# Kernel optimization log

Measured on AMD Instinct MI355X. Metric: run time of the kernel, lower is better.

Reference implementation:

```python
import jax, jax.numpy as jnp
import numpy as np

THETA = 10.0      # neuron['theta']
TAU_SR = 10.0     # neuron['tauSr']
TAU_REF = 1.0     # neuron['tauRef']
SCALE_REF = 2.0   # neuron['scaleRef']
TAU_RHO = 1.0     # neuron['tauRho']
SCALE_RHO = 1.0   # neuron['scaleRho']
EPS = 0.01        # kernel truncation epsilon
TS = 1.0          # simulation['Ts']
T_SAMPLE = 256    # time steps == seq_len (forward sets tSample = embed_out.size(1))


def _alpha_kernel(tau, mult):
    # slayerPytorch _calculateAlphaKernel: mult * t/tau * exp(1 - t/tau), truncated
    ker = []
    for t in np.arange(0.0, T_SAMPLE * TS, TS):
        v = mult * t / tau * np.exp(1.0 - t / tau)
        if abs(v) < EPS and t > tau:
            break
        ker.append(v)
    return np.asarray(ker, dtype=np.float32)


def psp(x, srm_kernel):
    # Causal temporal filter: out[t] = Ts * sum_k srm[k] * x[t-k];  x: (B, C, T)
    B, C, T = x.shape
    K = srm_kernel.shape[0]
    lhs = x.reshape(B * C, 1, T)
    rhs = srm_kernel[::-1].reshape(1, 1, K)  # reverse: correlation -> convolution
    out = jax.lax.conv_general_dilated(lhs, rhs, (1,), [(K - 1, 0)])
    return out.reshape(B, C, T) * TS


def _spike_scan(u, ref_kernel):
    # Sequential threshold with refractory feedback (SLAYER getSpikes). u: (B, C, T)
    B, C, T = u.shape
    future = ref_kernel[1:]  # ref_kernel[0] == 0, so spike at t only affects t+1..
    R = future.shape[0]

    def step(r, u_t):
        m = u_t + r[..., 0]                       # membrane incl. past refractory
        s = (m >= THETA).astype(u.dtype)
        r = jnp.concatenate([r[..., 1:], jnp.zeros_like(r[..., :1])], axis=-1)
        r = r + s[..., None] * future             # schedule refractory response
        return r, (s, m)

    r0 = jnp.zeros((B, C, R), u.dtype)
    _, (s, m) = jax.lax.scan(step, r0, jnp.moveaxis(u, -1, 0))
    return jnp.moveaxis(s, 0, -1), jnp.moveaxis(m, 0, -1)


@jax.custom_vjp
def spike(u, ref_kernel):
    return _spike_scan(u, ref_kernel)[0]


def _spike_fwd(u, ref_kernel):
    s, m = _spike_scan(u, ref_kernel)
    return s, (m, ref_kernel)


def _spike_bwd(res, g):
    # SLAYER surrogate gradient: straight-through pdf on post-refractory membrane
    m, ref_kernel = res
    tau = TAU_RHO * THETA
    pdf = (SCALE_RHO / tau) * jnp.exp(-jnp.abs(m - THETA) / tau)
    return g * pdf, jnp.zeros_like(ref_kernel)


spike.defvjp(_spike_fwd, _spike_bwd)


def setup_inputs() -> dict:
    key = jax.random.key(0)
    k1, k2, k3, k4 = jax.random.split(key, 4)
    VOCAB, EMB, HID, OUT, B = 50000, 300, 512, 10, 64
    feed_data = jax.random.randint(k1, (B, T_SAMPLE), 0, VOCAB)
    emb_weight = jax.random.normal(k2, (VOCAB, EMB), jnp.float32)
    W1 = jax.random.normal(k3, (HID, EMB), jnp.float32) * (4.0 / np.sqrt(EMB))
    W2 = jax.random.normal(k4, (OUT, HID), jnp.float32) * (4.0 / np.sqrt(HID))
    return {
        "feed_data": feed_data,
        "emb_weight": emb_weight,
        "W1": W1,
        "W2": W2,
        "srm_kernel": jnp.asarray(_alpha_kernel(TAU_SR, 1.0)),
        "ref_kernel": jnp.asarray(_alpha_kernel(TAU_REF, -SCALE_REF * THETA)),
    }


def reference(feed_data, emb_weight, W1, W2, srm_kernel, ref_kernel):
    x = emb_weight[feed_data]                 # (B, T, E); dropout = identity (eval)
    x = jnp.transpose(x, (0, 2, 1))           # (B, E, T) -- transpose(1,2)
    h = jnp.einsum('he,bet->bht', W1, x)      # slayer.dense == 1x1x1 conv3d, no bias
    h = spike(psp(h, srm_kernel), ref_kernel)
    o = jnp.einsum('oh,bht->bot', W2, h)
    return spike(psp(o, srm_kernel), ref_kernel)  # (B, OUT, T)
```

## Files before the change

### kernel.cpp

```cpp
#include <hip/hip_runtime.h>

#define BB    64
#define TT    256
#define EMBD  300
#define HIDD  512
#define OUTC  10
#define THETA 10.0
#define FUTN  12
#define KSMAX 80
#define HSTRIDE 344

__device__ __forceinline__ int hswz(int tt) { return tt ^ ((tt >> 4) & 7); }

__global__ __launch_bounds__(256)
void prep_kernel(const int* __restrict__ feed, const float* __restrict__ emb,
                 const float* __restrict__ W2, float* __restrict__ xg,
                 double* __restrict__ w2d)
{
    if (blockIdx.y == 8) {
        const int k = blockIdx.x * 256 + threadIdx.x;
        if (k < OUTC * HIDD) w2d[k] = (double)W2[k];
        return;
    }
    __shared__ float xt[32][305];
    __shared__ int   idx32[32];
    const int tid = threadIdx.x;
    const int b   = blockIdx.x;
    const int t0  = blockIdx.y * 32;

    if (tid < 32) idx32[tid] = feed[b * TT + t0 + tid];
    __syncthreads();
    for (int t = tid >> 6; t < 32; t += 4) {
        const size_t row = (size_t)idx32[t] * EMBD;
        for (int e = (tid & 63); e < EMBD; e += 64)
            xt[t][e] = emb[row + e];
    }
    __syncthreads();
    const int tl = tid & 7;
    for (int e = tid >> 3; e < EMBD; e += 32) {
        float4 v;
        v.x = xt[4 * tl + 0][e];
        v.y = xt[4 * tl + 1][e];
        v.z = xt[4 * tl + 2][e];
        v.w = xt[4 * tl + 3][e];
        *(float4*)&xg[((size_t)b * EMBD + e) * TT + t0 + 4 * tl] = v;
    }
}

__global__ __launch_bounds__(256, 3)
void layer1_kernel(const float* __restrict__ xg, const float* __restrict__ W1,
                   const float* __restrict__ srm, const float* __restrict__ refk,
                   unsigned char* __restrict__ s1, int Ks, int Kr)
{
    __shared__ union {
        float  x[16 * 260];
        double h[16 * HSTRIDE];
    } A;
    __shared__ union {
        double        w[16 * 34];
        unsigned char s[16 * 260];
    } B;
    __shared__ double srm_sm[KSMAX];

    const int tid = threadIdx.x;
    const int b   = blockIdx.x;
    const int c0  = blockIdx.y * 16;

    if (tid < KSMAX) srm_sm[tid] = (tid < Ks) ? (double)srm[tid] : 0.0;

    const int cg = tid & 3,  tg = tid >> 2;
    const int tl = tid & 63, wv = tid >> 6;
    const int ew = tid & 15, cw = tid >> 4;

    double acc[4][4];
#pragma unroll
    for (int i = 0; i < 4; ++i)
#pragma unroll
        for (int j = 0; j < 4; ++j) acc[i][j] = 0.0;

    float xr[4][4];
    float wr = 0.f;

    {
#pragma unroll
        for (int r = 0; r < 4; ++r)
            *(float4*)xr[r] = *(const float4*)&xg[((size_t)b * EMBD + 4 * wv + r) * TT + 4 * tl];
        wr = W1[(size_t)(c0 + cw) * EMBD + ew];
#pragma unroll
        for (int r = 0; r < 4; ++r)
            *(float4*)&A.x[(4 * wv + r) * 260 + 4 * tl] = *(float4*)xr[r];
        B.w[ew * 34 + cw] = (double)wr;
    }
    __syncthreads();

    const int NCH = (EMBD + 15) / 16;
    for (int ch = 0; ch < NCH; ++ch) {
        const int ecur = min(16, EMBD - ch * 16);
        const int e0n  = (ch + 1) * 16;
        const int ecn  = EMBD - e0n;
        if (ch + 1 < NCH) {
#pragma unroll
            for (int r = 0; r < 4; ++r) {
                const int e = 4 * wv + r;
                if (e < ecn)
                    *(float4*)xr[r] = *(const float4*)&xg[((size_t)b * EMBD + e0n + e) * TT + 4 * tl];
            }
            if (ew < ecn) wr = W1[(size_t)(c0 + cw) * EMBD + e0n + ew];
        }
        const float*  xp = &A.x[4 * tg];
        const double* wp = &B.w[4 * cg];
#pragma unroll 4
        for (int e = 0; e < ecur; ++e) {
            const float4  xv = *(const float4*)xp;
            const double2 wa = *(const double2*)wp;
            const double2 wb = *(const double2*)(wp + 2);
            const double xd0 = (double)xv.x, xd1 = (double)xv.y;
            const double xd2 = (double)xv.z, xd3 = (double)xv.w;
            acc[0][0] = fma(xd0, wa.x, acc[0][0]);
            acc[0][1] = fma(xd0, wa.y, acc[0][1]);
            acc[0][2] = fma(xd0, wb.x, acc[0][2]);
            acc[0][3] = fma(xd0, wb.y, acc[0][3]);
            acc[1][0] = fma(xd1, wa.x, acc[1][0]);
            acc[1][1] = fma(xd1, wa.y, acc[1][1]);
            acc[1][2] = fma(xd1, wb.x, acc[1][2]);
            acc[1][3] = fma(xd1, wb.y, acc[1][3]);
            acc[2][0] = fma(xd2, wa.x, acc[2][0]);
            acc[2][1] = fma(xd2, wa.y, acc[2][1]);
            acc[2][2] = fma(xd2, wb.x, acc[2][2]);
            acc[2][3] = fma(xd2, wb.y, acc[2][3]);
            acc[3][0] = fma(xd3, wa.x, acc[3][0]);
            acc[3][1] = fma(xd3, wa.y, acc[3][1]);
            acc[3][2] = fma(xd3, wb.x, acc[3][2]);
            acc[3][3] = fma(xd3, wb.y, acc[3][3]);
            xp += 260;
            wp += 34;
        }
        __syncthreads();
        if (ch + 1 < NCH) {
#pragma unroll
            for (int r = 0; r < 4; ++r) {
                const int e = 4 * wv + r;
                if (e < ecn)
                    *(float4*)&A.x[e * 260 + 4 * tl] = *(float4*)xr[r];
            }
            if (ew < ecn) B.w[ew * 34 + cw] = (double)wr;
            __syncthreads();
        }
    }

    const int cf = tid & 15, tb = tid >> 4;
    if (tb < 5) {
#pragma unroll
        for (int k = 0; k < 16; ++k)
            A.h[cf * HSTRIDE + hswz(tb * 16 + k)] = 0.0;
    }
#pragma unroll
    for (int i = 0; i < 4; ++i)
#pragma unroll
        for (int j = 0; j < 4; ++j)
            A.h[(4 * cg + j) * HSTRIDE + hswz(80 + 4 * tg + i)] = acc[i][j];
    __syncthreads();

    const int t0f = tb * 16;
    double* hrow = &A.h[cf * HSTRIDE];
    double p[16], win[16];
#pragma unroll
    for (int k = 0; k < 16; ++k) {
        p[k]   = 0.0;
        win[k] = hrow[hswz(80 + t0f + k)];
    }
    for (int jb = 0; jb < KSMAX; jb += 16) {
#pragma unroll
        for (int jj = 0; jj < 16; ++jj) {
            const double sj = srm_sm[jb + jj];
#pragma unroll
            for (int i = 0; i < 16; ++i)
                p[i] = fma(win[(16 + i - jj) & 15], sj, p[i]);
            win[(15 - jj) & 15] = hrow[hswz(80 + t0f - (jb + jj) - 1)];
        }
    }
    __syncthreads();
#pragma unroll
    for (int i = 0; i < 16; ++i)
        hrow[hswz(80 + t0f + i)] = p[i];
    __syncthreads();

    if (tid < 16) {
        double fut[FUTN], rsh[FUTN];
#pragma unroll
        for (int i = 0; i < FUTN; ++i) {
            fut[i] = (i + 1 < Kr) ? (double)refk[i + 1] : 0.0;
            rsh[i] = 0.0;
        }
        const double*  hr = &A.h[tid * HSTRIDE];
        unsigned char* sr = &B.s[tid * 260];
        for (int t = 0; t < TT; ++t) {
            const double m  = hr[hswz(80 + t)] + rsh[0];
            const double sv = (m >= THETA) ? 1.0 : 0.0;
#pragma unroll
            for (int i = 0; i < FUTN - 1; ++i) rsh[i] = fma(sv, fut[i], rsh[i + 1]);
            rsh[FUTN - 1] = sv * fut[FUTN - 1];
            sr[t] = (unsigned char)(sv != 0.0 ? 1 : 0);
        }
    }
    __syncthreads();

    {
        const int tl2 = tid & 63;
#pragma unroll
        for (int r = 0; r < 4; ++r) {
            const int c = (tid >> 6) + 4 * r;
            const unsigned int v = *(const unsigned int*)&B.s[c * 260 + 4 * tl2];
            *(unsigned int*)&s1[((size_t)b * HIDD + c0 + c) * TT + 4 * tl2] = v;
        }
    }
}

__global__ __launch_bounds__(256)
void layer2_kernel(const unsigned char* __restrict__ s1,
                   const double* __restrict__ w2d,
                   const float* __restrict__ srm, const float* __restrict__ refk,
                   float* __restrict__ out, int Ks, int Kr)
{
    __shared__ double        h2[OUTC * HSTRIDE];
    __shared__ unsigned char s2[OUTC * 260];
    __shared__ double        srm_sm[KSMAX];

    const int tid = threadIdx.x;
    const int b   = blockIdx.x;

    if (tid < KSMAX) srm_sm[tid] = (tid < Ks) ? (double)srm[tid] : 0.0;

    double acc[OUTC];
#pragma unroll
    for (int oc = 0; oc < OUTC; ++oc) acc[oc] = 0.0;

    const unsigned char* sp = s1 + (size_t)b * HIDD * TT + tid;
#pragma unroll 8
    for (int h = 0; h < HIDD; ++h) {
        const double sv = (double)sp[(size_t)h * TT];
#pragma unroll
        for (int oc = 0; oc < OUTC; ++oc)
            acc[oc] = fma(sv, w2d[oc * HIDD + h], acc[oc]);
    }

    const int cf = tid & 15, tb = tid >> 4;
    if (cf < OUTC && tb < 5) {
#pragma unroll
        for (int k = 0; k < 16; ++k)
            h2[cf * HSTRIDE + hswz(tb * 16 + k)] = 0.0;
    }
#pragma unroll
    for (int oc = 0; oc < OUTC; ++oc)
        h2[oc * HSTRIDE + hswz(80 + tid)] = acc[oc];
    __syncthreads();

    double p[16], win[16];
    double* hrow = &h2[cf * HSTRIDE];
    const int t0f = tb * 16;
    if (cf < OUTC) {
#pragma unroll
        for (int k = 0; k < 16; ++k) {
            p[k]   = 0.0;
            win[k] = hrow[hswz(80 + t0f + k)];
        }
        for (int jb = 0; jb < KSMAX; jb += 16) {
#pragma unroll
            for (int jj = 0; jj < 16; ++jj) {
                const double sj = srm_sm[jb + jj];
#pragma unroll
                for (int i = 0; i < 16; ++i)
                    p[i] = fma(win[(16 + i - jj) & 15], sj, p[i]);
                win[(15 - jj) & 15] = hrow[hswz(80 + t0f - (jb + jj) - 1)];
            }
        }
    }
    __syncthreads();
    if (cf < OUTC) {
#pragma unroll
        for (int i = 0; i < 16; ++i)
            hrow[hswz(80 + t0f + i)] = p[i];
    }
    __syncthreads();

    if (tid < OUTC) {
        double fut[FUTN], rsh[FUTN];
#pragma unroll
        for (int i = 0; i < FUTN; ++i) {
            fut[i] = (i + 1 < Kr) ? (double)refk[i + 1] : 0.0;
            rsh[i] = 0.0;
        }
        const double*  hr = &h2[tid * HSTRIDE];
        unsigned char* sr = &s2[tid * 260];
        for (int t = 0; t < TT; ++t) {
            const double m  = hr[hswz(80 + t)] + rsh[0];
            const double sv = (m >= THETA) ? 1.0 : 0.0;
#pragma unroll
            for (int i = 0; i < FUTN - 1; ++i) rsh[i] = fma(sv, fut[i], rsh[i + 1]);
            rsh[FUTN - 1] = sv * fut[FUTN - 1];
            sr[t] = (unsigned char)(sv != 0.0 ? 1 : 0);
        }
    }
    __syncthreads();

#pragma unroll
    for (int r = 0; r < OUTC; ++r)
        out[((size_t)b * OUTC + r) * TT + tid] = (float)s2[r * 260 + tid];
}

extern "C" void kernel_launch(void* const* d_in, const int* in_sizes, int n_in,
                              void* d_out, int out_size, void* d_ws, size_t ws_size,
                              hipStream_t stream)
{
    const int*   feed = (const int*)  d_in[0];
    const float* emb  = (const float*)d_in[1];
    const float* W1   = (const float*)d_in[2];
    const float* W2   = (const float*)d_in[3];
    const float* srm  = (const float*)d_in[4];
    const float* refk = (const float*)d_in[5];
    const int Ks = in_sizes[4];
    const int Kr = in_sizes[5];

    unsigned char* s1c = (unsigned char*)d_ws;
    float*  xg  = (float*) ((char*)d_ws + 8388608);
    double* w2d = (double*)((char*)d_ws + 8388608 + 19660800);
    float*  out = (float*)d_out;

    prep_kernel  <<<dim3(BB, 9),  256, 0, stream>>>(feed, emb, W2, xg, w2d);
    layer1_kernel<<<dim3(BB, 32), 256, 0, stream>>>(xg, W1, srm, refk, s1c, Ks, Kr);
    layer2_kernel<<<dim3(BB),     256, 0, stream>>>(s1c, w2d, srm, refk, out, Ks, Kr);
}
```

Before: 382.9 us.

## Split layer2 into parallel matvec and PSP kernels; store x as double in LDS

The single-block-per-batch layer2 kernel is split in two. layer2a spreads the 512-wide hidden reduction over 4 time quarters and 4 hidden slices per block, using LDS-staged W2 and a shared-memory reduction. layer2b does the PSP and spike scan on the reduced membrane. Layer1 now converts x to double once when staging into LDS instead of in the inner FMA loop. It also drops the swizzled padded h layout in favour of bounds-checked indexing and raises the occupancy hint from 3 to 4. The cost is an extra launch plus a global round trip for the intermediate m2, and more LDS for the double-precision x tile.

Result: slower. 659.4 us (+72.2%).

```diff
diff --git a/kernel.cpp b/kernel.cpp
--- a/kernel.cpp
+++ b/kernel.cpp
@@ -8,9 +8,8 @@
 #define THETA 10.0
 #define FUTN  12
 #define KSMAX 80
-#define HSTRIDE 344
-
-__device__ __forceinline__ int hswz(int tt) { return tt ^ ((tt >> 4) & 7); }
+#define XSTR  260
+#define HSTR  265
 
 __global__ __launch_bounds__(256)
 void prep_kernel(const int* __restrict__ feed, const float* __restrict__ emb,
@@ -47,19 +46,13 @@
     }
 }
 
-__global__ __launch_bounds__(256, 3)
+__global__ __launch_bounds__(256, 4)
 void layer1_kernel(const float* __restrict__ xg, const float* __restrict__ W1,
                    const float* __restrict__ srm, const float* __restrict__ refk,
                    unsigned char* __restrict__ s1, int Ks, int Kr)
 {
-    __shared__ union {
-        float  x[16 * 260];
-        double h[16 * HSTRIDE];
-    } A;
-    __shared__ union {
-        double        w[16 * 34];
-        unsigned char s[16 * 260];
-    } B;
+    __shared__ union { double x[16 * XSTR]; double h[16 * HSTR]; } A;
+    __shared__ union { double w[16 * 18]; unsigned char s[16 * 260]; } B;
     __shared__ double srm_sm[KSMAX];
 
     const int tid = threadIdx.x;
@@ -78,19 +71,20 @@
 #pragma unroll
         for (int j = 0; j < 4; ++j) acc[i][j] = 0.0;
 
-    float xr[4][4];
-    float wr = 0.f;
-
-    {
-#pragma unroll
-        for (int r = 0; r < 4; ++r)
-            *(float4*)xr[r] = *(const float4*)&xg[((size_t)b * EMBD + 4 * wv + r) * TT + 4 * tl];
-        wr = W1[(size_t)(c0 + cw) * EMBD + ew];
-#pragma unroll
-        for (int r = 0; r < 4; ++r)
-            *(float4*)&A.x[(4 * wv + r) * 260 + 4 * tl] = *(float4*)xr[r];
-        B.w[ew * 34 + cw] = (double)wr;
-    }
+    float4 xr[4];
+    float  wr = 0.f;
+
+#pragma unroll
+    for (int r = 0; r < 4; ++r)
+        xr[r] = *(const float4*)&xg[((size_t)b * EMBD + 4 * wv + r) * TT + 4 * tl];
+    wr = W1[(size_t)(c0 + cw) * EMBD + ew];
+#pragma unroll
+    for (int r = 0; r < 4; ++r) {
+        double* d = &A.x[(4 * wv + r) * XSTR + 4 * tl];
+        d[0] = (double)xr[r].x; d[1] = (double)xr[r].y;
+        d[2] = (double)xr[r].z; d[3] = (double)xr[r].w;
+    }
+    B.w[ew * 18 + cw] = (double)wr;
     __syncthreads();
 
     const int NCH = (EMBD + 15) / 16;
@@ -103,86 +97,87 @@
             for (int r = 0; r < 4; ++r) {
                 const int e = 4 * wv + r;
                 if (e < ecn)
-                    *(float4*)xr[r] = *(const float4*)&xg[((size_t)b * EMBD + e0n + e) * TT + 4 * tl];
+                    xr[r] = *(const float4*)&xg[((size_t)b * EMBD + e0n + e) * TT + 4 * tl];
             }
             if (ew < ecn) wr = W1[(size_t)(c0 + cw) * EMBD + e0n + ew];
         }
-        const float*  xp = &A.x[4 * tg];
+        const double* xp = &A.x[4 * tg];
         const double* wp = &B.w[4 * cg];
 #pragma unroll 4
         for (int e = 0; e < ecur; ++e) {
-            const float4  xv = *(const float4*)xp;
-            const double2 wa = *(const double2*)wp;
-            const double2 wb = *(const double2*)(wp + 2);
-            const double xd0 = (double)xv.x, xd1 = (double)xv.y;
-            const double xd2 = (double)xv.z, xd3 = (double)xv.w;
-            acc[0][0] = fma(xd0, wa.x, acc[0][0]);
-            acc[0][1] = fma(xd0, wa.y, acc[0][1]);
-            acc[0][2] = fma(xd0, wb.x, acc[0][2]);
-            acc[0][3] = fma(xd0, wb.y, acc[0][3]);
-            acc[1][0] = fma(xd1, wa.x, acc[1][0]);
-            acc[1][1] = fma(xd1, wa.y, acc[1][1]);
-            acc[1][2] = fma(xd1, wb.x, acc[1][2]);
-            acc[1][3] = fma(xd1, wb.y, acc[1][3]);
-            acc[2][0] = fma(xd2, wa.x, acc[2][0]);
-            acc[2][1] = fma(xd2, wa.y, acc[2][1]);
-            acc[2][2] = fma(xd2, wb.x, acc[2][2]);
-            acc[2][3] = fma(xd2, wb.y, acc[2][3]);
-            acc[3][0] = fma(xd3, wa.x, acc[3][0]);
-            acc[3][1] = fma(xd3, wa.y, acc[3][1]);
-            acc[3][2] = fma(xd3, wb.x, acc[3][2]);
-            acc[3][3] = fma(xd3, wb.y, acc[3][3]);
-            xp += 260;
-            wp += 34;
+            const double2 x01 = *(const double2*)xp;
+            const double2 x23 = *(const double2*)(xp + 2);
+            const double2 wa  = *(const double2*)wp;
+            const double2 wb  = *(const double2*)(wp + 2);
+            acc[0][0] = fma(x01.x, wa.x, acc[0][0]);
+            acc[0][1] = fma(x01.x, wa.y, acc[0][1]);
+            acc[0][2] = fma(x01.x, wb.x, acc[0][2]);
+            acc[0][3] = fma(x01.x, wb.y, acc[0][3]);
+            acc[1][0] = fma(x01.y, wa.x, acc[1][0]);
+            acc[1][1] = fma(x01.y, wa.y, acc[1][1]);
+            acc[1][2] = fma(x01.y, wb.x, acc[1][2]);
+            acc[1][3] = fma(x01.y, wb.y, acc[1][3]);
+            acc[2][0] = fma(x23.x, wa.x, acc[2][0]);
+            acc[2][1] = fma(x23.x, wa.y, acc[2][1]);
+            acc[2][2] = fma(x23.x, wb.x, acc[2][2]);
+            acc[2][3] = fma(x23.x, wb.y, acc[2][3]);
+            acc[3][0] = fma(x23.y, wa.x, acc[3][0]);
+            acc[3][1] = fma(x23.y, wa.y, acc[3][1]);
+            acc[3][2] = fma(x23.y, wb.x, acc[3][2]);
+            acc[3][3] = fma(x23.y, wb.y, acc[3][3]);
+            xp += XSTR;
+            wp += 18;
         }
         __syncthreads();
         if (ch + 1 < NCH) {
 #pragma unroll
             for (int r = 0; r < 4; ++r) {
                 const int e = 4 * wv + r;
-                if (e < ecn)
-                    *(float4*)&A.x[e * 260 + 4 * tl] = *(float4*)xr[r];
+                if (e < ecn) {
+                    double* d = &A.x[e * XSTR + 4 * tl];
+                    d[0] = (double)xr[r].x; d[1] = (double)xr[r].y;
+                    d[2] = (double)xr[r].z; d[3] = (double)xr[r].w;
+                }
             }
-            if (ew < ecn) B.w[ew * 34 + cw] = (double)wr;
+            if (ew < ecn) B.w[ew * 18 + cw] = (double)wr;
             __syncthreads();
         }
     }
 
+#pragma unroll
+    for (int i = 0; i < 4; ++i)
+#pragma unroll
+        for (int j = 0; j < 4; ++j)
+            A.h[(4 * cg + j) * HSTR + (4 * tg + i)] = acc[i][j];
+    __syncthreads();
+
     const int cf = tid & 15, tb = tid >> 4;
-    if (tb < 5) {
-#pragma unroll
-        for (int k = 0; k < 16; ++k)
-            A.h[cf * HSTRIDE + hswz(tb * 16 + k)] = 0.0;
-    }
-#pragma unroll
-    for (int i = 0; i < 4; ++i)
-#pragma unroll
-        for (int j = 0; j < 4; ++j)
-            A.h[(4 * cg + j) * HSTRIDE + hswz(80 + 4 * tg + i)] = acc[i][j];
-    __syncthreads();
-
-    const int t0f = tb * 16;
-    double* hrow = &A.h[cf * HSTRIDE];
-    double p[16], win[16];
-#pragma unroll
-    for (int k = 0; k < 16; ++k) {
-        p[k]   = 0.0;
-        win[k] = hrow[hswz(80 + t0f + k)];
-    }
-    for (int jb = 0; jb < KSMAX; jb += 16) {
-#pragma unroll
-        for (int jj = 0; jj < 16; ++jj) {
-            const double sj = srm_sm[jb + jj];
-#pragma unroll
-            for (int i = 0; i < 16; ++i)
-                p[i] = fma(win[(16 + i - jj) & 15], sj, p[i]);
-            win[(15 - jj) & 15] = hrow[hswz(80 + t0f - (jb + jj) - 1)];
-        }
-    }
-    __syncthreads();
-#pragma unroll
-    for (int i = 0; i < 16; ++i)
-        hrow[hswz(80 + t0f + i)] = p[i];
+    const double* hrow = &A.h[cf * HSTR];
+    double pout[16];
+#pragma unroll
+    for (int k = 0; k < 16; ++k) pout[k] = 0.0;
+#pragma unroll
+    for (int pp = 0; pp < 2; ++pp) {
+        const int t0 = tb * 16 + pp * 8;
+        double win[8];
+#pragma unroll
+        for (int k = 0; k < 8; ++k) win[k] = hrow[t0 + k];
+        for (int jb = 0; jb < KSMAX; jb += 8) {
+#pragma unroll
+            for (int jj = 0; jj < 8; ++jj) {
+                const double sj = srm_sm[jb + jj];
+#pragma unroll
+                for (int i = 0; i < 8; ++i)
+                    pout[pp * 8 + i] = fma(win[(8 + i - jj) & 7], sj, pout[pp * 8 + i]);
+                const int idx = t0 - (jb + jj) - 1;
+                win[(7 - jj) & 7] = (idx >= 0) ? hrow[idx] : 0.0;
+            }
+        }
+    }
+    __syncthreads();
+#pragma unroll
+    for (int k = 0; k < 16; ++k)
+        A.h[cf * HSTR + tb * 16 + k] = pout[k];
     __syncthreads();
 
     if (tid < 16) {
@@ -192,10 +187,10 @@
             fut[i] = (i + 1 < Kr) ? (double)refk[i + 1] : 0.0;
             rsh[i] = 0.0;
         }
-        const double*  hr = &A.h[tid * HSTRIDE];
+        const double*  hr = &A.h[tid * HSTR];
         unsigned char* sr = &B.s[tid * 260];
         for (int t = 0; t < TT; ++t) {
-            const double m  = hr[hswz(80 + t)] + rsh[0];
+            const double m  = hr[t] + rsh[0];
             const double sv = (m >= THETA) ? 1.0 : 0.0;
 #pragma unroll
             for (int i = 0; i < FUTN - 1; ++i) rsh[i] = fma(sv, fut[i], rsh[i + 1]);
@@ -217,70 +212,76 @@
 }
 
 __global__ __launch_bounds__(256)
-void layer2_kernel(const unsigned char* __restrict__ s1,
-                   const double* __restrict__ w2d,
-                   const float* __restrict__ srm, const float* __restrict__ refk,
-                   float* __restrict__ out, int Ks, int Kr)
-{
-    __shared__ double        h2[OUTC * HSTRIDE];
-    __shared__ unsigned char s2[OUTC * 260];
-    __shared__ double        srm_sm[KSMAX];
+void layer2a_kernel(const unsigned char* __restrict__ s1,
+                    const double* __restrict__ w2d, double* __restrict__ m2)
+{
+    __shared__ double w2l[OUTC * HIDD];
+    __shared__ double red[4][OUTC][65];
+
+    const int tid = threadIdx.x;
+    const int b = blockIdx.x, q = blockIdx.y;
+    const int tl = tid & 63, hq = tid >> 6;
+    const int t  = q * 64 + tl;
+
+    for (int u = tid; u < OUTC * HIDD; u += 256) w2l[u] = w2d[u];
+    __syncthreads();
+
+    double p[OUTC];
+#pragma unroll
+    for (int oc = 0; oc < OUTC; ++oc) p[oc] = 0.0;
+
+    const unsigned char* sp = s1 + ((size_t)b * HIDD + hq * 128) * TT + t;
+    for (int h0 = 0; h0 < 128; ++h0) {
+        const double sv = (double)sp[(size_t)h0 * TT];
+        const int h = hq * 128 + h0;
+#pragma unroll
+        for (int oc = 0; oc < OUTC; ++oc)
+            p[oc] = fma(sv, w2l[oc * HIDD + h], p[oc]);
+    }
+#pragma unroll
+    for (int oc = 0; oc < OUTC; ++oc) red[hq][oc][tl] = p[oc];
+    __syncthreads();
+
+    for (int u = tid; u < OUTC * 64; u += 256) {
+        const int oc = u >> 6, t2 = u & 63;
+        const double s = ((red[0][oc][t2] + red[1][oc][t2]) +
+                          red[2][oc][t2]) + red[3][oc][t2];
+        m2[((size_t)b * OUTC + oc) * TT + q * 64 + t2] = s;
+    }
+}
+
+__global__ __launch_bounds__(256)
+void layer2b_kernel(const double* __restrict__ m2, const float* __restrict__ srm,
+                    const float* __restrict__ refk, float* __restrict__ out,
+                    int Ks, int Kr)
+{
+    __shared__ double mh[OUTC][257];
+    __shared__ double uh[OUTC][257];
+    __shared__ double srm_sm[KSMAX];
+    __shared__ unsigned char s2[OUTC][260];
 
     const int tid = threadIdx.x;
     const int b   = blockIdx.x;
 
     if (tid < KSMAX) srm_sm[tid] = (tid < Ks) ? (double)srm[tid] : 0.0;
-
-    double acc[OUTC];
-#pragma unroll
-    for (int oc = 0; oc < OUTC; ++oc) acc[oc] = 0.0;
-
-    const unsigned char* sp = s1 + (size_t)b * HIDD * TT + tid;
-#pragma unroll 8
-    for (int h = 0; h < HIDD; ++h) {
-        const double sv = (double)sp[(size_t)h * TT];
-#pragma unroll
-        for (int oc = 0; oc < OUTC; ++oc)
-            acc[oc] = fma(sv, w2d[oc * HIDD + h], acc[oc]);
-    }
-
-    const int cf = tid & 15, tb = tid >> 4;
-    if (cf < OUTC && tb < 5) {
-#pragma unroll
-        for (int k = 0; k < 16; ++k)
-            h2[cf * HSTRIDE + hswz(tb * 16 + k)] = 0.0;
-    }
-#pragma unroll
-    for (int oc = 0; oc < OUTC; ++oc)
-        h2[oc * HSTRIDE + hswz(80 + tid)] = acc[oc];
-    __syncthreads();
-
-    double p[16], win[16];
-    double* hrow = &h2[cf * HSTRIDE];
-    const int t0f = tb * 16;
-    if (cf < OUTC) {
-#pragma unroll
-        for (int k = 0; k < 16; ++k) {
-            p[k]   = 0.0;
-            win[k] = hrow[hswz(80 + t0f + k)];
-        }
-        for (int jb = 0; jb < KSMAX; jb += 16) {
-#pragma unroll
-            for (int jj = 0; jj < 16; ++jj) {
-                const double sj = srm_sm[jb + jj];
-#pragma unroll
-                for (int i = 0; i < 16; ++i)
-                    p[i] = fma(win[(16 + i - jj) & 15], sj, p[i]);
-                win[(15 - jj) & 15] = hrow[hswz(80 + t0f - (jb + jj) - 1)];
-            }
-        }
-    }
-    __syncthreads();
-    if (cf < OUTC) {
-#pragma unroll
-        for (int i = 0; i < 16; ++i)
-            hrow[hswz(80 + t0f + i)] = p[i];
-    }
+    for (int u = tid; u < OUTC * TT; u += 256)
+        mh[u >> 8][u & 255] = m2[(size_t)b * OUTC * TT + u];
+    __syncthreads();
+
+    double p[OUTC];
+#pragma unroll
+    for (int oc = 0; oc < OUTC; ++oc) p[oc] = 0.0;
+    for (int j = 0; j < KSMAX; ++j) {
+        const int idx = tid - j;
+        if (idx >= 0) {
+            const double sj = srm_sm[j];
+#pragma unroll
+            for (int oc = 0; oc < OUTC; ++oc)
+                p[oc] = fma(mh[oc][idx], sj, p[oc]);
+        }
+    }
+#pragma unroll
+    for (int oc = 0; oc < OUTC; ++oc) uh[oc][tid] = p[oc];
     __syncthreads();
 
     if (tid < OUTC) {
@@ -290,22 +291,19 @@
             fut[i] = (i + 1 < Kr) ? (double)refk[i + 1] : 0.0;
             rsh[i] = 0.0;
         }
-        const double*  hr = &h2[tid * HSTRIDE];
-        unsigned char* sr = &s2[tid * 260];
         for (int t = 0; t < TT; ++t) {
-            const double m  = hr[hswz(80 + t)] + rsh[0];
+            const double m  = uh[tid][t] + rsh[0];
             const double sv = (m >= THETA) ? 1.0 : 0.0;
 #pragma unroll
             for (int i = 0; i < FUTN - 1; ++i) rsh[i] = fma(sv, fut[i], rsh[i + 1]);
             rsh[FUTN - 1] = sv * fut[FUTN - 1];
-            sr[t] = (unsigned char)(sv != 0.0 ? 1 : 0);
-        }
-    }
-    __syncthreads();
-
-#pragma unroll
-    for (int r = 0; r < OUTC; ++r)
-        out[((size_t)b * OUTC + r) * TT + tid] = (float)s2[r * 260 + tid];
+            s2[tid][t] = (unsigned char)(sv != 0.0 ? 1 : 0);
+        }
+    }
+    __syncthreads();
+
+    for (int u = tid; u < OUTC * TT; u += 256)
+        out[(size_t)b * OUTC * TT + u] = (float)s2[u >> 8][u & 255];
 }
 
 extern "C" void kernel_launch(void* const* d_in, const int* in_sizes, int n_in,
@@ -323,10 +321,12 @@
 
     unsigned char* s1c = (unsigned char*)d_ws;
     float*  xg  = (float*) ((char*)d_ws + 8388608);
+    double* m2  = (double*)((char*)d_ws + 8388608);
     double* w2d = (double*)((char*)d_ws + 8388608 + 19660800);
     float*  out = (float*)d_out;
 
-    prep_kernel  <<<dim3(BB, 9),  256, 0, stream>>>(feed, emb, W2, xg, w2d);
-    layer1_kernel<<<dim3(BB, 32), 256, 0, stream>>>(xg, W1, srm, refk, s1c, Ks, Kr);
-    layer2_kernel<<<dim3(BB),     256, 0, stream>>>(s1c, w2d, srm, refk, out, Ks, Kr);
-}
+    prep_kernel   <<<dim3(BB, 9),  256, 0, stream>>>(feed, emb, W2, xg, w2d);
+    layer1_kernel <<<dim3(BB, 32), 256, 0, stream>>>(xg, W1, srm, refk, s1c, Ks, Kr);
+    layer2a_kernel<<<dim3(BB, 4),  256, 0, stream>>>(s1c, w2d, m2);
+    layer2b_kernel<<<dim3(BB),     256, 0, stream>>>(m2, srm, refk, out, Ks, Kr);
+}
```
